# Kernel tuning notes

Measured on AMD Instinct MI355X. Metric: run time of the kernel, lower is better.

## Reference

```python
import jax, jax.numpy as jnp
import numpy as np

DECAY = 0.99
EPS = 1e-5
K = 1024  # num_embeddings
D = 64    # embedding_dim


def setup_inputs() -> dict:
    key = jax.random.key(0)
    k1, k2 = jax.random.split(key)
    inputs = jax.random.normal(k1, (64, 64, 32, 32), dtype=jnp.float32)
    weight = jax.random.uniform(k2, (K, D), minval=-1.0 / K, maxval=1.0 / K, dtype=jnp.float32)
    cluster_size = jnp.zeros((K,), dtype=jnp.float32)
    embed_avg = weight.copy()
    return {"inputs": inputs, "weight": weight, "cluster_size": cluster_size, "embed_avg": embed_avg}


def reference(inputs, weight, cluster_size, embed_avg):
    B, _, H, W = inputs.shape
    # faithful to torch: raw memory-order view(-1, D), no channel permute
    flat = inputs.reshape(-1, D)  # (N, D), N = B*H*W
    distances = (jnp.sum(flat * flat, axis=1, keepdims=True)
                 + jnp.sum(weight * weight, axis=1)
                 - 2.0 * flat @ weight.T)
    idx = jnp.argmin(distances, axis=1)  # (N,)
    quantized = weight[idx].reshape(inputs.shape)  # == onehot @ weight, reshaped

    # EMA codebook update (training path)
    counts = jax.ops.segment_sum(jnp.ones(flat.shape[0], dtype=jnp.float32), idx, num_segments=K)
    cs = DECAY * cluster_size + (1.0 - DECAY) * counts
    n = jnp.sum(cs)
    cs = (cs + EPS) / (n + K * EPS) * n
    dw = jax.ops.segment_sum(flat, idx, num_segments=K)  # == onehot^T @ flat
    new_embed_avg = DECAY * embed_avg + (1.0 - DECAY) * dw
    new_weight = new_embed_avg / cs[:, None]

    # straight-through estimator
    quantized_st = inputs + jax.lax.stop_gradient(quantized - inputs)
    indices = idx.reshape(B, H, W)
    return quantized_st, indices, new_weight, cs, new_embed_avg
```

## Files before the change

### kernel.cpp

```cpp
#include <hip/hip_runtime.h>

#define NROWS 65536
#define KC    1024
#define DD    64

#define QOFF  0
#define IOFF  4194304
#define WOFF  4259840
#define CSOFF 4325376
#define EAOFF 4326400

#define WS_CODESQ  0
#define WS_COUNTS  1056
#define WS_RCCNT   2080
#define WS_CURSOR  2096
#define WS_OFFS    3120
#define WS_CSFIN   4144
#define WS_DW      5168
#define WS_WSWZ    70704
#define WS_IDX     137264
#define WS_RCLIST  202800
#define WS_ROWLIST 268336
#define WS_PACKED  333872

#define MARGIN 5e-5f

typedef _Float16 half8 __attribute__((ext_vector_type(8)));
typedef float    floatx4 __attribute__((ext_vector_type(4)));

struct F4 { float x, y, z, w; };
typedef const __attribute__((address_space(4))) F4    c4F4;
typedef const __attribute__((address_space(4))) float c4f;

__device__ __forceinline__ unsigned f2ord(float f) {
    unsigned u = __float_as_uint(f);
    return (u & 0x80000000u) ? ~u : (u | 0x80000000u);
}

__device__ __forceinline__ float med3f(float a, float b, float c) {
    float d;
    asm("v_med3_f32 %0, %1, %2, %3" : "=v"(d) : "v"(a), "v"(b), "v"(c));
    return d;
}

__device__ __forceinline__ float rowsq4(const float4* xv) {
    float4 re, ro;
    re.x = __fmul_rn(xv[0].x, xv[0].x); re.y = __fmul_rn(xv[0].y, xv[0].y);
    re.z = __fmul_rn(xv[0].z, xv[0].z); re.w = __fmul_rn(xv[0].w, xv[0].w);
    ro.x = __fmul_rn(xv[1].x, xv[1].x); ro.y = __fmul_rn(xv[1].y, xv[1].y);
    ro.z = __fmul_rn(xv[1].z, xv[1].z); ro.w = __fmul_rn(xv[1].w, xv[1].w);
#pragma unroll
    for (int i = 2; i < 16; i += 2) {
        re.x = __fadd_rn(re.x, __fmul_rn(xv[i].x, xv[i].x));
        re.y = __fadd_rn(re.y, __fmul_rn(xv[i].y, xv[i].y));
        re.z = __fadd_rn(re.z, __fmul_rn(xv[i].z, xv[i].z));
        re.w = __fadd_rn(re.w, __fmul_rn(xv[i].w, xv[i].w));
        ro.x = __fadd_rn(ro.x, __fmul_rn(xv[i + 1].x, xv[i + 1].x));
        ro.y = __fadd_rn(ro.y, __fmul_rn(xv[i + 1].y, xv[i + 1].y));
        ro.z = __fadd_rn(ro.z, __fmul_rn(xv[i + 1].z, xv[i + 1].z));
        ro.w = __fadd_rn(ro.w, __fmul_rn(xv[i + 1].w, xv[i + 1].w));
    }
    return __fadd_rn(__fadd_rn(__fadd_rn(re.x, re.y), __fadd_rn(re.z, re.w)),
                     __fadd_rn(__fadd_rn(ro.x, ro.y), __fadd_rn(ro.z, ro.w)));
}

__global__ void prep_kernel(const float* __restrict__ weight,
                            float* __restrict__ code_sq,
                            _Float16* __restrict__ wswz,
                            float* __restrict__ counts,
                            int* __restrict__ rccnt) {
    int c = blockIdx.x * blockDim.x + threadIdx.x;
    if (c >= KC) return;
    counts[c] = 0.0f;
    if (c == 0) rccnt[0] = 0;
    float4 wv4[16];
    const float4* pw = reinterpret_cast<const float4*>(weight + (size_t)c * DD);
#pragma unroll
    for (int i = 0; i < 16; ++i) wv4[i] = pw[i];
    code_sq[c] = rowsq4(wv4);
    float w64[64];
#pragma unroll
    for (int i = 0; i < 16; ++i) {
        w64[4 * i] = wv4[i].x; w64[4 * i + 1] = wv4[i].y;
        w64[4 * i + 2] = wv4[i].z; w64[4 * i + 3] = wv4[i].w;
    }
    const int t32 = c >> 5;
    const int s16 = (c >> 4) & 1;
    const int cl  = c & 15;
    const size_t base = (size_t)t32 * 4096 + s16 * 2048 + cl * 8;
#pragma unroll
    for (int q = 0; q < 8; ++q) {
        half8 h, l;
#pragma unroll
        for (int j = 0; j < 8; ++j) {
            float s = w64[q * 8 + j] * 1024.0f;
            _Float16 hh = (_Float16)s;
            h[j] = hh;
            l[j] = (_Float16)(s - (float)hh);
        }
        *reinterpret_cast<half8*>(wswz + base + q * 128)        = h;
        *reinterpret_cast<half8*>(wswz + base + 1024 + q * 128) = l;
    }
}

__global__ __launch_bounds__(256, 4) void vq_scan(
    const float* __restrict__ x_in, const float* __restrict__ code_sq,
    const _Float16* __restrict__ wswz,
    float* __restrict__ out, float* __restrict__ counts,
    int* __restrict__ idxbuf, int* __restrict__ rccnt, int* __restrict__ rclist,
    unsigned long long* __restrict__ packed) {

    __shared__ __align__(16) _Float16 lds_b[2][8192];
    __shared__ float lds_csq[KC];
    __shared__ float sm1[4][32], sm2[4][32];
    __shared__ int   si1[4][32];

    const int tid  = threadIdx.x;
    const int lane = tid & 63;
    const int w    = tid >> 6;
    const int wm   = w & 1;
    const int wsel = w >> 1;
    const int l15  = lane & 15;
    const int g    = lane >> 4;

    const int blockRow0 = blockIdx.x * 64;
    const int waveRow0  = blockRow0 + wm * 32;

    char* gsrc0 = const_cast<char*>(reinterpret_cast<const char*>(wswz));

#pragma unroll
    for (int j = 0; j < 4; ++j) {
        __builtin_amdgcn_global_load_lds(
            (__attribute__((address_space(1))) void*)(gsrc0 + tid * 16 + j * 4096),
            (__attribute__((address_space(3))) void*)((char*)lds_b[0] + tid * 16 + j * 4096),
            16, 0, 0);
    }

#pragma unroll
    for (int i = 0; i < 4; ++i) lds_csq[tid + i * 256] = code_sq[tid + i * 256];

    half8 ah[4], al[4];
#pragma unroll
    for (int t = 0; t < 2; ++t) {
#pragma unroll
        for (int kh = 0; kh < 2; ++kh) {
            const float4* p4 = reinterpret_cast<const float4*>(
                x_in + (size_t)(waveRow0 + t * 16 + l15) * DD + kh * 32 + g * 8);
            float4 v0 = p4[0], v1 = p4[1];
            float vals[8] = {v0.x, v0.y, v0.z, v0.w, v1.x, v1.y, v1.z, v1.w};
            half8 hh, ll;
#pragma unroll
            for (int j = 0; j < 8; ++j) {
                _Float16 h = (_Float16)vals[j];
                hh[j] = h;
                ll[j] = (_Float16)(vals[j] - (float)h);
            }
            ah[t * 2 + kh] = hh;
            al[t * 2 + kh] = ll;
        }
    }
    __syncthreads();

    float m1[2][4], m2[2][4];
    int   i1[2][4];
#pragma unroll
    for (int t = 0; t < 2; ++t)
#pragma unroll
        for (int r = 0; r < 4; ++r) { m1[t][r] = INFINITY; m2[t][r] = INFINITY; i1[t][r] = 0; }

    int cur = 0;
    for (int p = 0; p < 16; ++p) {
        if (p < 15) {
            char* src = gsrc0 + (size_t)(p + 1) * 16384;
            char* dst = (char*)lds_b[cur ^ 1];
#pragma unroll
            for (int j = 0; j < 4; ++j) {
                __builtin_amdgcn_global_load_lds(
                    (__attribute__((address_space(1))) void*)(src + tid * 16 + j * 4096),
                    (__attribute__((address_space(3))) void*)(dst + tid * 16 + j * 4096),
                    16, 0, 0);
            }
        }

#pragma unroll
        for (int half = 0; half < 2; ++half) {
            const _Float16* S = lds_b[cur] + half * 4096 + wsel * 2048;
            half8 bh0 = *reinterpret_cast<const half8*>(S + g * 128 + l15 * 8);
            half8 bh1 = *reinterpret_cast<const half8*>(S + 512 + g * 128 + l15 * 8);
            half8 bl0 = *reinterpret_cast<const half8*>(S + 1024 + g * 128 + l15 * 8);
            half8 bl1 = *reinterpret_cast<const half8*>(S + 1536 + g * 128 + l15 * 8);
            const int code = p * 64 + half * 32 + wsel * 16 + l15;
            const float csq = lds_csq[code];
#pragma unroll
            for (int t = 0; t < 2; ++t) {
                floatx4 c1 = {0.f, 0.f, 0.f, 0.f};
                floatx4 c2 = {0.f, 0.f, 0.f, 0.f};
                c1 = __builtin_amdgcn_mfma_f32_16x16x32_f16(al[t * 2 + 0], bh0, c1, 0, 0, 0);
                c2 = __builtin_amdgcn_mfma_f32_16x16x32_f16(al[t * 2 + 1], bh1, c2, 0, 0, 0);
                c1 = __builtin_amdgcn_mfma_f32_16x16x32_f16(ah[t * 2 + 0], bl0, c1, 0, 0, 0);
                c2 = __builtin_amdgcn_mfma_f32_16x16x32_f16(ah[t * 2 + 1], bl1, c2, 0, 0, 0);
                c1 = __builtin_amdgcn_mfma_f32_16x16x32_f16(ah[t * 2 + 0], bh0, c1, 0, 0, 0);
                c2 = __builtin_amdgcn_mfma_f32_16x16x32_f16(ah[t * 2 + 1], bh1, c2, 0, 0, 0);
#pragma unroll
                for (int r = 0; r < 4; ++r) {
                    float s = fmaf(c1[r] + c2[r], -0x1p-9f, csq);
                    float mo = m1[t][r];
                    m2[t][r] = med3f(s, mo, m2[t][r]);
                    i1[t][r] = (s < mo) ? code : i1[t][r];
                    m1[t][r] = fminf(mo, s);
                }
            }
        }

        __syncthreads();
        cur ^= 1;
    }

#pragma unroll
    for (int t = 0; t < 2; ++t)
#pragma unroll
        for (int r = 0; r < 4; ++r)
#pragma unroll
            for (int mk = 1; mk < 16; mk <<= 1) {
                float o1 = __shfl_xor(m1[t][r], mk);
                float o2 = __shfl_xor(m2[t][r], mk);
                int   oi = __shfl_xor(i1[t][r], mk);
                float n2 = fminf(fminf(m2[t][r], o2), fmaxf(m1[t][r], o1));
                bool sel = (o1 < m1[t][r]) || (o1 == m1[t][r] && oi < i1[t][r]);
                m1[t][r] = sel ? o1 : m1[t][r];
                i1[t][r] = sel ? oi : i1[t][r];
                m2[t][r] = n2;
            }

    if (l15 == 0) {
#pragma unroll
        for (int t = 0; t < 2; ++t)
#pragma unroll
            for (int r = 0; r < 4; ++r) {
                int rib = t * 16 + g * 4 + r;
                sm1[w][rib] = m1[t][r];
                sm2[w][rib] = m2[t][r];
                si1[w][rib] = i1[t][r];
            }
    }
    __syncthreads();

    if (tid < 64) {
        int pwm = tid >> 5;
        int rib = tid & 31;
        float bm1 = sm1[pwm][rib], bm2 = sm2[pwm][rib];
        int bi = si1[pwm][rib];
        {
            float v1 = sm1[pwm + 2][rib];
            float v2 = sm2[pwm + 2][rib];
            int   vi = si1[pwm + 2][rib];
            if (v1 < bm1 || (v1 == bm1 && vi < bi)) {
                bm2 = fminf(bm1, v2);
                bm1 = v1; bi = vi;
            } else {
                bm2 = fminf(bm2, v1);
            }
        }
        int grow = blockRow0 + pwm * 32 + rib;
        if (bm2 - bm1 >= MARGIN) {
            idxbuf[grow] = bi;
            out[IOFF + grow] = (float)bi;
            atomicAdd(&counts[bi], 1.0f);
        } else {
            packed[grow] = 0xFFFFFFFFFFFFFFFFull;
            int pos = atomicAdd(rccnt, 1);
            rclist[pos] = grow;
        }
    }
}

__global__ __launch_bounds__(256, 4) void vq_recheck(
    const float* __restrict__ x_in, const float* __restrict__ weight,
    const float* __restrict__ code_sq,
    unsigned long long* __restrict__ packed,
    const int* __restrict__ rccnt, const int* __restrict__ rclist) {

    const int nrc = rccnt[0];
    const int nitems = ((nrc + 63) >> 6) * 16;

    const int tid  = threadIdx.x;
    const int lane = tid & 63;
    const int wvu  = __builtin_amdgcn_readfirstlane(tid >> 6);

    for (int item = blockIdx.x; item < nitems; item += gridDim.x) {
        const int rb     = (item >> 4) * 64;
        const int cchunk = item & 15;
        const bool valid = (rb + lane) < nrc;
        const int  grow  = rclist[valid ? rb + lane : rb];

        float4 xv[16];
        const float4* px = reinterpret_cast<const float4*>(x_in + (size_t)grow * DD);
#pragma unroll
        for (int i = 0; i < 16; ++i) xv[i] = px[i];
        const float rs = rowsq4(xv);

        const int k0 = cchunk * 64 + wvu * 16;
        unsigned long long wa = (unsigned long long)(weight + (size_t)k0 * DD);
        unsigned long long ca = (unsigned long long)(code_sq + k0);
        unsigned wal = __builtin_amdgcn_readfirstlane((unsigned)wa);
        unsigned wah = __builtin_amdgcn_readfirstlane((unsigned)(wa >> 32));
        unsigned cal = __builtin_amdgcn_readfirstlane((unsigned)ca);
        unsigned cah = __builtin_amdgcn_readfirstlane((unsigned)(ca >> 32));
        c4F4* wb4 = (c4F4*)(((unsigned long long)wah << 32) | wal);
        c4f*  cb  = (c4f*)(((unsigned long long)cah << 32) | cal);

        float best = INFINITY;
        int bidx = 0x7fffffff;

#pragma unroll 2
        for (int k = 0; k < 16; ++k) {
            float a0 = 0.f, a1 = 0.f, a2 = 0.f, a3 = 0.f;
#pragma unroll
            for (int i = 0; i < 16; ++i) {
                F4 w4;
                w4.x = wb4[k * 16 + i].x;
                w4.y = wb4[k * 16 + i].y;
                w4.z = wb4[k * 16 + i].z;
                w4.w = wb4[k * 16 + i].w;
                a0 += xv[i].x * w4.x;
                a1 += xv[i].y * w4.y;
                a2 += xv[i].z * w4.z;
                a3 += xv[i].w * w4.w;
            }
            float dot = (a0 + a1) + (a2 + a3);
            float csq = cb[k];
            float dst = __fsub_rn(__fadd_rn(rs, csq), __fmul_rn(2.0f, dot));
            int kg = k0 + k;
            if (dst < best) { best = dst; bidx = kg; }
        }

        if (valid) {
            unsigned long long p =
                ((unsigned long long)f2ord(best) << 32) | (unsigned)bidx;
            atomicMin(&packed[grow], p);
        }
    }
}

__global__ void rc_offsets_cs(const unsigned long long* __restrict__ packed,
                              const int* __restrict__ rccnt,
                              const int* __restrict__ rclist,
                              const float* __restrict__ cluster_size,
                              float* __restrict__ out, int* __restrict__ idxbuf,
                              float* __restrict__ counts,
                              int* __restrict__ offs, int* __restrict__ cursor,
                              float* __restrict__ cs_fin) {
    __shared__ int   hist[1024];
    __shared__ int   sc[1024];
    __shared__ float sb[1024];
    int k = threadIdx.x;
    hist[k] = 0;
    __syncthreads();
    const int nrc = rccnt[0];
    for (int i = k; i < nrc; i += 1024) {
        int grow = rclist[i];
        int bidx = (int)(packed[grow] & 0xFFFFFFFFull);
        out[IOFF + grow] = (float)bidx;
        idxbuf[grow] = bidx;
        atomicAdd(&hist[bidx], 1);
    }
    __syncthreads();
    int c = (int)counts[k] + hist[k];
    counts[k] = (float)c;
    float ce = 0.99f * cluster_size[k] + 0.01f * (float)c;
    sc[k] = c;
    sb[k] = ce;
    __syncthreads();
    for (int off = 1; off < 1024; off <<= 1) {
        int v = (k >= off) ? sc[k - off] : 0;
        __syncthreads();
        sc[k] += v;
        __syncthreads();
    }
    offs[k] = sc[k] - c;
    cursor[k] = 0;
    for (int off = 512; off > 0; off >>= 1) {
        if (k < off) sb[k] += sb[k + off];
        __syncthreads();
    }
    float n = sb[0];
    float v = ((ce + 1e-5f) / (n + 0.01024f)) * n;
    out[CSOFF + k] = v;
    cs_fin[k] = v;
}

__global__ void scatter_kernel(const int* __restrict__ idxbuf,
                               const int* __restrict__ offs,
                               int* __restrict__ cursor,
                               int* __restrict__ rowlist) {
    int r = blockIdx.x * blockDim.x + threadIdx.x;
    if (r >= NROWS) return;
    int k = idxbuf[r];
    int pos = atomicAdd(&cursor[k], 1);
    rowlist[offs[k] + pos] = r;
}

__global__ __launch_bounds__(512) void dw_q_kernel(
    const float* __restrict__ x_in,
    const float* __restrict__ weight,
    const float* __restrict__ counts,
    const int* __restrict__ offs,
    const int* __restrict__ rowlist,
    const float* __restrict__ embed_avg,
    const float* __restrict__ cs_fin,
    float* __restrict__ out, float* __restrict__ dw) {
    __shared__ float wsh[64];
    __shared__ float part[8][64];

    const int k    = blockIdx.x;
    const int tid  = threadIdx.x;
    const int lane = tid & 63;
    const int wv   = tid >> 6;

    if (tid < 64) wsh[tid] = weight[(size_t)k * DD + tid];
    __syncthreads();

    const int cnt  = (int)counts[k];
    const int base = offs[k];
    const float wk = wsh[lane];

    float acc = 0.f;
    int i = wv;
    for (; i + 24 < cnt; i += 32) {
        int r0 = rowlist[base + i];
        int r1 = rowlist[base + i + 8];
        int r2 = rowlist[base + i + 16];
        int r3 = rowlist[base + i + 24];
        float x0 = x_in[(size_t)r0 * DD + lane];
        float x1 = x_in[(size_t)r1 * DD + lane];
        float x2 = x_in[(size_t)r2 * DD + lane];
        float x3 = x_in[(size_t)r3 * DD + lane];
        out[QOFF + (size_t)r0 * DD + lane] = __fadd_rn(x0, __fsub_rn(wk, x0));
        out[QOFF + (size_t)r1 * DD + lane] = __fadd_rn(x1, __fsub_rn(wk, x1));
        out[QOFF + (size_t)r2 * DD + lane] = __fadd_rn(x2, __fsub_rn(wk, x2));
        out[QOFF + (size_t)r3 * DD + lane] = __fadd_rn(x3, __fsub_rn(wk, x3));
        acc = __fadd_rn(acc, x0);
        acc = __fadd_rn(acc, x1);
        acc = __fadd_rn(acc, x2);
        acc = __fadd_rn(acc, x3);
    }
    for (; i < cnt; i += 8) {
        int r = rowlist[base + i];
        float xq = x_in[(size_t)r * DD + lane];
        out[QOFF + (size_t)r * DD + lane] = __fadd_rn(xq, __fsub_rn(wk, xq));
        acc = __fadd_rn(acc, xq);
    }
    part[wv][lane] = acc;
    __syncthreads();
    if (tid < 64) {
        float s01 = __fadd_rn(part[0][tid], part[1][tid]);
        float s23 = __fadd_rn(part[2][tid], part[3][tid]);
        float s45 = __fadd_rn(part[4][tid], part[5][tid]);
        float s67 = __fadd_rn(part[6][tid], part[7][tid]);
        float s = __fadd_rn(__fadd_rn(s01, s23), __fadd_rn(s45, s67));
        int e = k * DD + tid;
        dw[e] = s;
        float na = 0.99f * embed_avg[e] + 0.01f * s;
        out[EAOFF + e] = na;
        out[WOFF + e] = na / cs_fin[k];
    }
}

extern "C" void kernel_launch(void* const* d_in, const int* in_sizes, int n_in,
                              void* d_out, int out_size, void* d_ws, size_t ws_size,
                              hipStream_t stream) {
    (void)in_sizes; (void)n_in; (void)out_size; (void)ws_size;
    const float* x       = (const float*)d_in[0];
    const float* weight  = (const float*)d_in[1];
    const float* cluster = (const float*)d_in[2];
    const float* eavg    = (const float*)d_in[3];
    float* out = (float*)d_out;
    float* wsf = (float*)d_ws;

    float*    code_sq = wsf + WS_CODESQ;
    float*    counts  = wsf + WS_COUNTS;
    int*      rccnt   = (int*)(wsf + WS_RCCNT);
    int*      cursor  = (int*)(wsf + WS_CURSOR);
    int*      offs    = (int*)(wsf + WS_OFFS);
    float*    cs_fin  = wsf + WS_CSFIN;
    float*    dwbuf   = wsf + WS_DW;
    _Float16* wswz    = (_Float16*)(wsf + WS_WSWZ);
    int*      idxbuf  = (int*)(wsf + WS_IDX);
    int*      rclist  = (int*)(wsf + WS_RCLIST);
    int*      rowlist = (int*)(wsf + WS_ROWLIST);
    unsigned long long* packed = (unsigned long long*)(wsf + WS_PACKED);

    hipLaunchKernelGGL(prep_kernel, dim3(16), dim3(64), 0, stream,
                       weight, code_sq, wswz, counts, rccnt);
    hipLaunchKernelGGL(vq_scan, dim3(1024), dim3(256), 0, stream,
                       x, code_sq, wswz, out, counts, idxbuf, rccnt, rclist,
                       packed);
    hipLaunchKernelGGL(vq_recheck, dim3(2048), dim3(256), 0, stream,
                       x, weight, code_sq, packed, rccnt, rclist);
    hipLaunchKernelGGL(rc_offsets_cs, dim3(1), dim3(1024), 0, stream,
                       packed, rccnt, rclist, cluster, out, idxbuf, counts,
                       offs, cursor, cs_fin);
    hipLaunchKernelGGL(scatter_kernel, dim3(256), dim3(256), 0, stream,
                       idxbuf, offs, cursor, rowlist);
    hipLaunchKernelGGL(dw_q_kernel, dim3(1024), dim3(512), 0, stream,
                       x, weight, counts, offs, rowlist, eavg, cs_fin, out, dwbuf);
}
```

Baseline: 117.2 us.

## Write quantized output in scan kernel for decided rows, flag rows for dw pass

For rows whose argmin clears the margin, the scan kernel now writes the straight-through quantized output right away while x is likely still cached. A decided bit is tagged in idxbuf and carried through scatter into rowlist. dw_q_kernel then writes quantized values only for rows that went through recheck, which cuts its scattered global stores. In exchange the scan kernel gains an extra pass reading x and weight plus a barrier, and idx values carry a flag bit that must be masked everywhere they are read.

```diff
diff --git a/kernel.cpp b/kernel.cpp
--- a/kernel.cpp
+++ b/kernel.cpp
@@ -24,6 +24,7 @@
 #define WS_PACKED  333872
 
 #define MARGIN 5e-5f
+#define DECIDED_BIT 0x10000
 
 typedef _Float16 half8 __attribute__((ext_vector_type(8)));
 typedef float    floatx4 __attribute__((ext_vector_type(4)));
@@ -104,8 +105,8 @@
 }
 
 __global__ __launch_bounds__(256, 4) void vq_scan(
-    const float* __restrict__ x_in, const float* __restrict__ code_sq,
-    const _Float16* __restrict__ wswz,
+    const float* __restrict__ x_in, const float* __restrict__ weight,
+    const float* __restrict__ code_sq, const _Float16* __restrict__ wswz,
     float* __restrict__ out, float* __restrict__ counts,
     int* __restrict__ idxbuf, int* __restrict__ rccnt, int* __restrict__ rclist,
     unsigned long long* __restrict__ packed) {
@@ -114,6 +115,7 @@
     __shared__ float lds_csq[KC];
     __shared__ float sm1[4][32], sm2[4][32];
     __shared__ int   si1[4][32];
+    __shared__ int   idx_l[64];
 
     const int tid  = threadIdx.x;
     const int lane = tid & 63;
@@ -261,15 +263,41 @@
                 bm2 = fminf(bm2, v1);
             }
         }
-        int grow = blockRow0 + pwm * 32 + rib;
+        int grow = blockRow0 + tid;
         if (bm2 - bm1 >= MARGIN) {
-            idxbuf[grow] = bi;
+            idxbuf[grow] = bi | DECIDED_BIT;
             out[IOFF + grow] = (float)bi;
             atomicAdd(&counts[bi], 1.0f);
+            idx_l[tid] = bi;
         } else {
             packed[grow] = 0xFFFFFFFFFFFFFFFFull;
             int pos = atomicAdd(rccnt, 1);
             rclist[pos] = grow;
+            idx_l[tid] = -1;
+        }
+    }
+    __syncthreads();
+
+    {
+        const float4* xin4 = reinterpret_cast<const float4*>(x_in);
+        const float4* w4g  = reinterpret_cast<const float4*>(weight);
+        float4* q4 = reinterpret_cast<float4*>(out + QOFF);
+        const size_t blk4 = (size_t)blockRow0 * 16;
+#pragma unroll
+        for (int j = 0; j < 4; ++j) {
+            int f4i = tid + j * 256;
+            int rl  = f4i >> 4;
+            int d4  = f4i & 15;
+            int idx = idx_l[rl];
+            if (idx < 0) continue;
+            float4 xq = xin4[blk4 + f4i];
+            float4 wq = w4g[idx * 16 + d4];
+            float4 qv;
+            qv.x = __fadd_rn(xq.x, __fsub_rn(wq.x, xq.x));
+            qv.y = __fadd_rn(xq.y, __fsub_rn(wq.y, xq.y));
+            qv.z = __fadd_rn(xq.z, __fsub_rn(wq.z, xq.z));
+            qv.w = __fadd_rn(xq.w, __fsub_rn(wq.w, xq.w));
+            q4[blk4 + f4i] = qv;
         }
     }
 }
@@ -395,9 +423,10 @@
                                int* __restrict__ rowlist) {
     int r = blockIdx.x * blockDim.x + threadIdx.x;
     if (r >= NROWS) return;
-    int k = idxbuf[r];
+    int v = idxbuf[r];
+    int k = v & 1023;
     int pos = atomicAdd(&cursor[k], 1);
-    rowlist[offs[k] + pos] = r;
+    rowlist[offs[k] + pos] = r | ((v & DECIDED_BIT) ? 0 : 0x80000000);
 }
 
 __global__ __launch_bounds__(512) void dw_q_kernel(
@@ -427,27 +456,32 @@
     float acc = 0.f;
     int i = wv;
     for (; i + 24 < cnt; i += 32) {
-        int r0 = rowlist[base + i];
-        int r1 = rowlist[base + i + 8];
-        int r2 = rowlist[base + i + 16];
-        int r3 = rowlist[base + i + 24];
+        int e0 = rowlist[base + i];
+        int e1 = rowlist[base + i + 8];
+        int e2 = rowlist[base + i + 16];
+        int e3 = rowlist[base + i + 24];
+        int r0 = e0 & 0x7fffffff;
+        int r1 = e1 & 0x7fffffff;
+        int r2 = e2 & 0x7fffffff;
+        int r3 = e3 & 0x7fffffff;
         float x0 = x_in[(size_t)r0 * DD + lane];
         float x1 = x_in[(size_t)r1 * DD + lane];
         float x2 = x_in[(size_t)r2 * DD + lane];
         float x3 = x_in[(size_t)r3 * DD + lane];
-        out[QOFF + (size_t)r0 * DD + lane] = __fadd_rn(x0, __fsub_rn(wk, x0));
-        out[QOFF + (size_t)r1 * DD + lane] = __fadd_rn(x1, __fsub_rn(wk, x1));
-        out[QOFF + (size_t)r2 * DD + lane] = __fadd_rn(x2, __fsub_rn(wk, x2));
-        out[QOFF + (size_t)r3 * DD + lane] = __fadd_rn(x3, __fsub_rn(wk, x3));
+        if (e0 < 0) out[QOFF + (size_t)r0 * DD + lane] = __fadd_rn(x0, __fsub_rn(wk, x0));
+        if (e1 < 0) out[QOFF + (size_t)r1 * DD + lane] = __fadd_rn(x1, __fsub_rn(wk, x1));
+        if (e2 < 0) out[QOFF + (size_t)r2 * DD + lane] = __fadd_rn(x2, __fsub_rn(wk, x2));
+        if (e3 < 0) out[QOFF + (size_t)r3 * DD + lane] = __fadd_rn(x3, __fsub_rn(wk, x3));
         acc = __fadd_rn(acc, x0);
         acc = __fadd_rn(acc, x1);
         acc = __fadd_rn(acc, x2);
         acc = __fadd_rn(acc, x3);
     }
     for (; i < cnt; i += 8) {
-        int r = rowlist[base + i];
+        int e = rowlist[base + i];
+        int r = e & 0x7fffffff;
         float xq = x_in[(size_t)r * DD + lane];
-        out[QOFF + (size_t)r * DD + lane] = __fadd_rn(xq, __fsub_rn(wk, xq));
+        if (e < 0) out[QOFF + (size_t)r * DD + lane] = __fadd_rn(xq, __fsub_rn(wk, xq));
         acc = __fadd_rn(acc, xq);
     }
     part[wv][lane] = acc;
@@ -493,8 +527,8 @@
     hipLaunchKernelGGL(prep_kernel, dim3(16), dim3(64), 0, stream,
                        weight, code_sq, wswz, counts, rccnt);
     hipLaunchKernelGGL(vq_scan, dim3(1024), dim3(256), 0, stream,
-                       x, code_sq, wswz, out, counts, idxbuf, rccnt, rclist,
-                       packed);
+                       x, weight, code_sq, wswz, out, counts, idxbuf, rccnt,
+                       rclist, packed);
     hipLaunchKernelGGL(vq_recheck, dim3(2048), dim3(256), 0, stream,
                        x, weight, code_sq, packed, rccnt, rclist);
     hipLaunchKernelGGL(rc_offsets_cs, dim3(1), dim3(1024), 0, stream,
```

New measurement: 115.8 us, median of 2. About the same (-1.2%).
